# Performance work log

Hardware: AMD Instinct MI355X
Metric: run time of the kernel (lower is better)

Reference implementation:

```python
import jax, jax.numpy as jnp
import numpy as np

# dimensions
B, NQ, D, H, L, KT, KF = 4, 8192, 256, 8, 4, 2, 2
K = KT * KF
DH = D // H
SPATIAL = np.array([[64, 64], [32, 32], [16, 16], [8, 8]], dtype=np.int32)  # (H_l, W_l)
_sizes = SPATIAL[:, 0] * SPATIAL[:, 1]
LSI = np.concatenate([[0], np.cumsum(_sizes)[:-1]]).astype(np.int32)
NV = int(_sizes.sum())


def setup_inputs() -> dict:
    key = jax.random.key(0)
    ks = jax.random.split(key, 12)
    s = 0.02  # small weight scale keeps tanh in linear region like the zero-init original
    # biases per _reset_parameters: +-0.5 grid for offsets, level-specialization for level_weights
    b_time = jnp.asarray(np.tile(np.linspace(-0.5, 0.5, KT), H * L).astype(np.float32))
    b_freq = jnp.asarray(np.tile(np.linspace(-0.5, 0.5, KF).astype(np.float32), H * L))
    lvl_bias = np.zeros((H, L), dtype=np.float32)
    hpl = max(1, H // L)
    for lvl in range(L):
        lvl_bias[lvl * hpl:min(lvl * hpl + hpl, H), lvl] = 1.0
    return dict(
        query=jax.random.normal(ks[0], (B, NQ, D), jnp.float32),
        reference_points=jax.random.uniform(ks[1], (B, NQ, L, 2), jnp.float32),
        value=jax.random.normal(ks[2], (B, NV, D), jnp.float32),
        spatial_shapes=jnp.asarray(SPATIAL),
        level_start_index=jnp.asarray(LSI),
        W_time=jax.random.normal(ks[3], (D, H * L * KT), jnp.float32) * s,
        b_time=b_time,
        W_freq=jax.random.normal(ks[4], (D, H * L * KF), jnp.float32) * s,
        b_freq=b_freq,
        W_lvl=jax.random.normal(ks[5], (D, H * L), jnp.float32) * s,
        b_lvl=jnp.asarray(lvl_bias.reshape(-1)),
        W_pt=jax.random.normal(ks[6], (D, H * L * K), jnp.float32) * s,
        b_pt=jnp.zeros((H * L * K,), jnp.float32),
        W_v=jax.random.normal(ks[7], (D, D), jnp.float32) * (1.0 / np.sqrt(D)),
        b_v=jnp.zeros((D,), jnp.float32),
        W_o=jax.random.normal(ks[8], (D, D), jnp.float32) * (1.0 / np.sqrt(D)),
        b_o=jnp.zeros((D,), jnp.float32),
    )


def _bilinear(vlev, gx, gy, Hl, Wl):
    # vlev: [B,H,Hl*Wl,DH]; gx,gy: [B,H,NQ,K] normalized grid coords in [-1,1]
    # F.grid_sample(align_corners=False, padding_mode='zeros') semantics
    x = (gx + 1.0) * (Wl * 0.5) - 0.5
    y = (gy + 1.0) * (Hl * 0.5) - 0.5
    x0 = jnp.floor(x)
    y0 = jnp.floor(y)
    wx1 = x - x0
    wy1 = y - y0
    x0i = x0.astype(jnp.int32)
    y0i = y0.astype(jnp.int32)

    def gather(xi, yi, w):
        valid = (xi >= 0) & (xi < Wl) & (yi >= 0) & (yi < Hl)
        idx = jnp.clip(yi, 0, Hl - 1) * Wl + jnp.clip(xi, 0, Wl - 1)
        b, h, nq, k = idx.shape
        v = jnp.take_along_axis(vlev, idx.reshape(b, h, nq * k)[..., None], axis=2)
        v = v.reshape(b, h, nq, k, DH)
        return v * (w * valid)[..., None]

    return (gather(x0i, y0i, (1.0 - wx1) * (1.0 - wy1))
            + gather(x0i + 1, y0i, wx1 * (1.0 - wy1))
            + gather(x0i, y0i + 1, (1.0 - wx1) * wy1)
            + gather(x0i + 1, y0i + 1, wx1 * wy1))


def _forward(query, reference_points, value, W_time, b_time, W_freq, b_freq,
             W_lvl, b_lvl, W_pt, b_pt, W_v, b_v, W_o, b_o,
             spatial_shapes, level_start_index):
    ss = np.asarray(spatial_shapes)
    lsi = np.asarray(level_start_index)
    # predicted separable offsets (offset_scale = 1.0)
    t_off = jnp.tanh(query @ W_time + b_time).reshape(B, NQ, H, L, KT)
    f_off = jnp.tanh(query @ W_freq + b_freq).reshape(B, NQ, H, L, KF)
    # square grid: outer product of time (x) and freq (y) offsets -> K = KT*KF points
    off = jnp.stack([
        jnp.broadcast_to(t_off[..., :, None], (B, NQ, H, L, KT, KF)),
        jnp.broadcast_to(f_off[..., None, :], (B, NQ, H, L, KT, KF)),
    ], axis=-1).reshape(B, NQ, H, L, K, 2)
    # normalizer: (W_l, H_l) per level
    norm = jnp.stack([spatial_shapes[:, 1], spatial_shapes[:, 0]], axis=-1).astype(jnp.float32)
    loc = reference_points[:, :, None, :, None, :] + off / norm[None, None, None, :, None, :]
    loc = jnp.clip(loc, 0.0, 1.0)
    grid = 2.0 * loc - 1.0  # [B,NQ,H,L,K,2], last dim = (x, y)
    # attention weights: softmax over levels times softmax over points
    lw = jax.nn.softmax((query @ W_lvl + b_lvl).reshape(B, NQ, H, L), axis=-1)
    pw = jax.nn.softmax((query @ W_pt + b_pt).reshape(B, NQ, H, L, K), axis=-1)
    attn = lw[..., None] * pw  # [B,NQ,H,L,K]
    v = (value @ W_v + b_v).reshape(B, NV, H, DH)
    out = jnp.zeros((B, NQ, H, DH), jnp.float32)
    for lid in range(L):
        Hl, Wl = int(ss[lid, 0]), int(ss[lid, 1])
        start = int(lsi[lid])
        vlev = v[:, start:start + Hl * Wl].transpose(0, 2, 1, 3)  # [B,H,S_l,DH]
        gx = grid[:, :, :, lid, :, 0].transpose(0, 2, 1, 3)  # [B,H,NQ,K]
        gy = grid[:, :, :, lid, :, 1].transpose(0, 2, 1, 3)
        sampled = _bilinear(vlev, gx, gy, Hl, Wl)  # [B,H,NQ,K,DH]
        a = attn[:, :, :, lid, :].transpose(0, 2, 1, 3)  # [B,H,NQ,K]
        out = out + jnp.einsum('bhqkd,bhqk->bqhd', sampled, a)
    out = out.reshape(B, NQ, D)
    return out @ W_o + b_o


def reference(query, reference_points, value, spatial_shapes, level_start_index,
              W_time, b_time, W_freq, b_freq, W_lvl, b_lvl, W_pt, b_pt,
              W_v, b_v, W_o, b_o):
    return _forward(query, reference_points, value, W_time, b_time, W_freq, b_freq,
                    W_lvl, b_lvl, W_pt, b_pt, W_v, b_v, W_o, b_o,
                    spatial_shapes, level_start_index)
```

## Files before the change

kernel.cpp:

```cpp
#include <hip/hip_runtime.h>
#include <math.h>

#define B_  4
#define NQ_ 8192
#define D_  256
#define H_  8
#define L_  4
#define K_  4
#define DH_ 32
#define NV_ 5440

#define SLAB_ 5936

typedef short bf16x8 __attribute__((ext_vector_type(8)));
typedef float f32x4  __attribute__((ext_vector_type(4)));
typedef float f32x8  __attribute__((ext_vector_type(8)));
typedef unsigned short u16x8 __attribute__((ext_vector_type(8)));

__device__ __forceinline__ ushort f2bf(float f) {
    union { float f; unsigned u; } v; v.f = f;
    return (ushort)((v.u + 0x7FFF + ((v.u >> 16) & 1)) >> 16);
}
__device__ __forceinline__ float bf2f(ushort u) {
    union { unsigned u; float f; } v; v.u = ((unsigned)u) << 16;
    return v.f;
}

__global__ __launch_bounds__(256) void k_prep(const float* __restrict__ Wv,
                                              const float* __restrict__ Wo,
                                              const float* __restrict__ Wt,
                                              const float* __restrict__ Wf,
                                              const float* __restrict__ Wlv,
                                              const float* __restrict__ Wp,
                                              uint4* __restrict__ vzero,
                                              ushort* __restrict__ Wvt,
                                              ushort* __restrict__ Wot,
                                              ushort* __restrict__ Wqt) {
    const int bk = blockIdx.x;
    const int t  = threadIdx.x;
    if (bk < 2968) {
        vzero[(size_t)bk * 256 + t] = make_uint4(0, 0, 0, 0);
    } else if (bk < 3480) {
        const float* in; ushort* out; int n;
        if (bk < 3224) { in = Wv; out = Wvt; n = bk - 2968; }
        else           { in = Wo; out = Wot; n = bk - 3224; }
        out[n * 256 + t] = f2bf(in[t * 256 + n]);
    } else {
        const int n = bk - 3480;
        float v;
        if (n < 64)       v = Wt[t * 64 + n];
        else if (n < 128) v = Wf[t * 64 + (n - 64)];
        else if (n < 160) v = Wlv[t * 32 + (n - 128)];
        else              v = Wp[t * 128 + (n - 160)];
        Wqt[n * 256 + t] = f2bf(v);
    }
}

template<int MODE, int AF32>
__global__ __launch_bounds__(256) void k_gemm(const void* __restrict__ Ap,
                                              const ushort* __restrict__ Bt,
                                              const float* __restrict__ bias,
                                              void* __restrict__ Cp) {
    constexpr int NT = 128;
    constexpr int NFN = 4;
    __shared__ ushort As[128 * 32];
    __shared__ ushort Bs[NT * 32];
    const int m0   = blockIdx.x * 128;
    const int n0   = blockIdx.y * NT;
    const int t    = threadIdx.x;
    const int w    = t >> 6;
    const int lane = t & 63;
    const int wm   = (w >> 1) * 64;
    const int wn   = (w & 1) * (NT / 2);
    const int lm   = lane & 15;
    const int quad = lane >> 4;

    f32x4 acc[4][NFN];
    #pragma unroll
    for (int i = 0; i < 4; ++i)
        #pragma unroll
        for (int j = 0; j < NFN; ++j)
            acc[i][j] = (f32x4)(0.f);

    for (int kc = 0; kc < 256; kc += 32) {
        __syncthreads();
        if (AF32) {
            const float* A = (const float*)Ap;
            #pragma unroll
            for (int i = 0; i < 4; ++i) {
                const int c   = t + i * 256;
                const int row = c >> 3, ko = (c & 7) * 4;
                const float4 v = *(const float4*)&A[(size_t)(m0 + row) * 256 + kc + ko];
                ushort4 u; u.x = f2bf(v.x); u.y = f2bf(v.y); u.z = f2bf(v.z); u.w = f2bf(v.w);
                *(ushort4*)&As[row * 32 + ko] = u;
            }
        } else {
            const ushort* A = (const ushort*)Ap;
            #pragma unroll
            for (int i = 0; i < 2; ++i) {
                const int c   = t + i * 256;
                const int row = c >> 2, ko = (c & 3) * 8;
                *(u16x8*)&As[row * 32 + ko] =
                    *(const u16x8*)&A[(size_t)(m0 + row) * 256 + kc + ko];
            }
        }
        #pragma unroll
        for (int i = 0; i < 2; ++i) {
            const int c = t + i * 256;
            const int row = c >> 2, ko = (c & 3) * 8;
            *(u16x8*)&Bs[row * 32 + ko] =
                *(const u16x8*)&Bt[(size_t)(n0 + row) * 256 + kc + ko];
        }
        __syncthreads();

        bf16x8 af[4], bfr[NFN];
        #pragma unroll
        for (int mf = 0; mf < 4; ++mf)
            af[mf] = *(const bf16x8*)&As[(wm + mf * 16 + lm) * 32 + quad * 8];
        #pragma unroll
        for (int nf = 0; nf < NFN; ++nf)
            bfr[nf] = *(const bf16x8*)&Bs[(wn + nf * 16 + lm) * 32 + quad * 8];
        #pragma unroll
        for (int mf = 0; mf < 4; ++mf)
            #pragma unroll
            for (int nf = 0; nf < NFN; ++nf)
                acc[mf][nf] = __builtin_amdgcn_mfma_f32_16x16x32_bf16(
                    af[mf], bfr[nf], acc[mf][nf], 0, 0, 0);
    }

    #pragma unroll
    for (int mf = 0; mf < 4; ++mf) {
        #pragma unroll
        for (int nf = 0; nf < NFN; ++nf) {
            const f32x4 a = acc[mf][nf];
            const int col   = n0 + wn + nf * 16 + lm;
            const int rbase = m0 + wm + mf * 16 + quad * 4;
            #pragma unroll
            for (int r = 0; r < 4; ++r) {
                const int row = rbase + r;
                const float v = a[r];
                if (MODE == 0) {
                    ((float*)Cp)[(size_t)row * 256 + col] = v + bias[col];
                } else {
                    const int b = row / NV_, s = row - b * NV_;
                    const int h = col >> 5, dh = col & 31;
                    const int l = (s >= 5376) ? 3 : (s >= 5120) ? 2 : (s >= 4096) ? 1 : 0;
                    const int lsi_[4] = {0, 4096, 5120, 5376};
                    const int po_[4]  = {0, 4356, 5512, 5836};
                    const int o  = s - lsi_[l];
                    const int Wl = 64 >> l;
                    const int y  = o >> (6 - l);
                    const int x  = o & (Wl - 1);
                    const int prow = po_[l] + (y + 1) * (Wl + 2) + (x + 1);
                    ((ushort*)Cp)[(((size_t)(b * H_ + h)) * SLAB_ + prow) * 32 + dh] =
                        f2bf(v + bias[col]);
                }
            }
        }
    }
}

__global__ __launch_bounds__(256) void k_qproj(const float* __restrict__ query,
                                               const ushort* __restrict__ Wqt,
                                               const float* __restrict__ refpts,
                                               const float* __restrict__ bt,
                                               const float* __restrict__ bfq,
                                               const float* __restrict__ blv,
                                               const float* __restrict__ bp,
                                               float* __restrict__ params) {
    __shared__ __align__(16) char smem[37888];
    ushort* As = (ushort*)smem;
    ushort* Bs = As + 64 * 32;
    float*  ep = (float*)smem;

    const int m0   = blockIdx.x * 64;
    const int t    = threadIdx.x;
    const int w    = t >> 6;
    const int lane = t & 63;
    const int wm   = (w >> 1) * 32;
    const int wn   = (w & 1) * 144;
    const int lm   = lane & 15;
    const int quad = lane >> 4;

    f32x4 acc[2][9];
    #pragma unroll
    for (int i = 0; i < 2; ++i)
        #pragma unroll
        for (int j = 0; j < 9; ++j)
            acc[i][j] = (f32x4)(0.f);

    for (int kc = 0; kc < 256; kc += 32) {
        __syncthreads();
        #pragma unroll
        for (int i = 0; i < 2; ++i) {
            const int c   = t + i * 256;
            const int row = c >> 3, ko = (c & 7) * 4;
            const float4 v = *(const float4*)&query[(size_t)(m0 + row) * 256 + kc + ko];
            ushort4 u; u.x = f2bf(v.x); u.y = f2bf(v.y); u.z = f2bf(v.z); u.w = f2bf(v.w);
            *(ushort4*)&As[row * 32 + ko] = u;
        }
        #pragma unroll
        for (int i = 0; i < 5; ++i) {
            const int c = t + i * 256;
            if (c < 1152) {
                const int row = c >> 2, ko = (c & 3) * 8;
                *(u16x8*)&Bs[row * 32 + ko] =
                    *(const u16x8*)&Wqt[(size_t)row * 256 + kc + ko];
            }
        }
        __syncthreads();

        bf16x8 af[2], bfr[9];
        #pragma unroll
        for (int mf = 0; mf < 2; ++mf)
            af[mf] = *(const bf16x8*)&As[(wm + mf * 16 + lm) * 32 + quad * 8];
        #pragma unroll
        for (int nf = 0; nf < 9; ++nf)
            bfr[nf] = *(const bf16x8*)&Bs[(wn + nf * 16 + lm) * 32 + quad * 8];
        #pragma unroll
        for (int mf = 0; mf < 2; ++mf)
            #pragma unroll
            for (int nf = 0; nf < 9; ++nf)
                acc[mf][nf] = __builtin_amdgcn_mfma_f32_16x16x32_bf16(
                    af[mf], bfr[nf], acc[mf][nf], 0, 0, 0);
    }

    #pragma unroll
    for (int ph = 0; ph < 2; ++ph) {
        __syncthreads();
        if ((w >> 1) == ph) {
            #pragma unroll
            for (int mf = 0; mf < 2; ++mf)
                #pragma unroll
                for (int nf = 0; nf < 9; ++nf)
                    #pragma unroll
                    for (int r = 0; r < 4; ++r)
                        ep[(mf * 16 + quad * 4 + r) * 296 + wn + nf * 16 + lm]
                            = acc[mf][nf][r];
        }
        __syncthreads();
        #pragma unroll
        for (int it = 0; it < 4; ++it) {
            const int item = t + it * 256;
            const int qr = item >> 5;
            const int hl = item & 31;
            const int h = hl >> 2, l = hl & 3;
            const int qg = m0 + ph * 32 + qr;
            const float* lgr = &ep[qr * 296];

            const float tA = tanhf(lgr[hl * 2 + 0] + bt[hl * 2 + 0]);
            const float tB = tanhf(lgr[hl * 2 + 1] + bt[hl * 2 + 1]);
            const float fA = tanhf(lgr[64 + hl * 2 + 0] + bfq[hl * 2 + 0]);
            const float fB = tanhf(lgr[64 + hl * 2 + 1] + bfq[hl * 2 + 1]);

            const float l0 = lgr[128 + h * 4 + 0] + blv[h * 4 + 0];
            const float l1 = lgr[128 + h * 4 + 1] + blv[h * 4 + 1];
            const float l2 = lgr[128 + h * 4 + 2] + blv[h * 4 + 2];
            const float l3 = lgr[128 + h * 4 + 3] + blv[h * 4 + 3];
            const float lmx = fmaxf(fmaxf(l0, l1), fmaxf(l2, l3));
            const float e0 = __expf(l0 - lmx), e1 = __expf(l1 - lmx);
            const float e2 = __expf(l2 - lmx), e3 = __expf(l3 - lmx);
            const float lsum = e0 + e1 + e2 + e3;
            const float lwv = ((l == 0) ? e0 : (l == 1) ? e1 : (l == 2) ? e2 : e3) / lsum;

            const float p0 = lgr[160 + hl * 4 + 0] + bp[hl * 4 + 0];
            const float p1 = lgr[160 + hl * 4 + 1] + bp[hl * 4 + 1];
            const float p2 = lgr[160 + hl * 4 + 2] + bp[hl * 4 + 2];
            const float p3 = lgr[160 + hl * 4 + 3] + bp[hl * 4 + 3];
            const float pmx = fmaxf(fmaxf(p0, p1), fmaxf(p2, p3));
            const float q0e = __expf(p0 - pmx), q1e = __expf(p1 - pmx);
            const float q2e = __expf(p2 - pmx), q3e = __expf(p3 - pmx);
            const float inv = lwv / (q0e + q1e + q2e + q3e);

            const float rx = refpts[((size_t)qg * L_ + l) * 2 + 0];
            const float ry = refpts[((size_t)qg * L_ + l) * 2 + 1];
            const float Wlf = (float)(64 >> l);
            const float Hlf = (float)(64 >> l);
            const float xA = fminf(fmaxf(rx + tA / Wlf, 0.f), 1.f) * Wlf - 0.5f;
            const float xB = fminf(fmaxf(rx + tB / Wlf, 0.f), 1.f) * Wlf - 0.5f;
            const float yA = fminf(fmaxf(ry + fA / Hlf, 0.f), 1.f) * Hlf - 0.5f;
            const float yB = fminf(fmaxf(ry + fB / Hlf, 0.f), 1.f) * Hlf - 0.5f;

            float* pp = params + (size_t)qg * 256 + hl * 8;
            pp[0] = q0e * inv; pp[1] = q1e * inv; pp[2] = q2e * inv; pp[3] = q3e * inv;
            pp[4] = xA; pp[5] = xB; pp[6] = yA; pp[7] = yB;
        }
    }
}

__global__ __launch_bounds__(256) void k_sample(const ushort* __restrict__ vperm,
                                                const float* __restrict__ params,
                                                ushort* __restrict__ mid) {
    __shared__ float pm[8][264];
    const int fid = blockIdx.x;
    const int b   = (fid & 7) >> 1;
    const int q0  = (((fid >> 3) << 1) | (fid & 1)) * 8;
    const int t   = threadIdx.x;
    const int ql  = t >> 5;
    const int sub = t & 31;
    const int h   = sub >> 2;
    const int dh8 = sub & 3;

    for (int i = t; i < 8 * 256; i += 256) {
        const int q = i >> 8, c = i & 255;
        pm[q][(c >> 5) * 33 + (c & 31)] = params[((size_t)(b * NQ_ + q0 + q)) * 256 + c];
    }
    __syncthreads();

    const ushort* vb = vperm + ((size_t)(b * H_ + h)) * SLAB_ * 32 + dh8 * 8;
    const int po_[4] = {0, 4356, 5512, 5836};

    f32x8 acc = (f32x8)(0.f);
    #pragma unroll
    for (int l = 0; l < L_; ++l) {
        const int W2 = (64 >> l) + 2;
        const ushort* vl = vb + (size_t)po_[l] * 32;
        const float* p  = &pm[ql][h * 33 + l * 8];
        const float a0 = p[0], a1 = p[1], a2 = p[2], a3 = p[3];
        const float xA = p[4], xB = p[5], yA = p[6], yB = p[7];
        const float xa0 = floorf(xA), xb0 = floorf(xB);
        const float ya0 = floorf(yA), yb0 = floorf(yB);
        const float fxa = xA - xa0, fxb = xB - xb0;
        const float fya = yA - ya0, fyb = yB - yb0;
        const int pxa = (int)xa0 + 1, pxb = (int)xb0 + 1;
        const int pya = (int)ya0 + 1, pyb = (int)yb0 + 1;
        #pragma unroll
        for (int k = 0; k < 4; ++k) {
            const int   px = (k & 2) ? pxb : pxa;
            const int   py = (k & 1) ? pyb : pya;
            const float fx = (k & 2) ? fxb : fxa;
            const float fy = (k & 1) ? fyb : fya;
            const float ak = (k == 0) ? a0 : (k == 1) ? a1 : (k == 2) ? a2 : a3;
            const ushort* cp = vl + (size_t)(py * W2 + px) * 32;
            const u16x8 u00 = *(const u16x8*)cp;
            const u16x8 u10 = *(const u16x8*)(cp + 32);
            const u16x8 u01 = *(const u16x8*)(cp + W2 * 32);
            const u16x8 u11 = *(const u16x8*)(cp + (W2 + 1) * 32);
            const float gx = 1.f - fx, gy = 1.f - fy;
            const float w00 = ak * gx * gy, w10 = ak * fx * gy;
            const float w01 = ak * gx * fy, w11 = ak * fx * fy;
            #pragma unroll
            for (int e = 0; e < 8; ++e)
                acc[e] += bf2f(u00[e]) * w00 + bf2f(u10[e]) * w10
                        + bf2f(u01[e]) * w01 + bf2f(u11[e]) * w11;
        }
    }
    u16x8 o;
    #pragma unroll
    for (int e = 0; e < 8; ++e) o[e] = f2bf(acc[e]);
    *(u16x8*)&mid[((size_t)(b * NQ_ + q0 + ql)) * 256 + sub * 8] = o;
}

extern "C" void kernel_launch(void* const* d_in, const int* in_sizes, int n_in,
                              void* d_out, int out_size, void* d_ws, size_t ws_size,
                              hipStream_t stream) {
    const float* query = (const float*)d_in[0];
    const float* refp  = (const float*)d_in[1];
    const float* value = (const float*)d_in[2];
    const float* Wt = (const float*)d_in[5];
    const float* bt = (const float*)d_in[6];
    const float* Wf = (const float*)d_in[7];
    const float* bf = (const float*)d_in[8];
    const float* Wl = (const float*)d_in[9];
    const float* bl = (const float*)d_in[10];
    const float* Wp = (const float*)d_in[11];
    const float* bp = (const float*)d_in[12];
    const float* Wv = (const float*)d_in[13];
    const float* bv = (const float*)d_in[14];
    const float* Wo = (const float*)d_in[15];
    const float* bo = (const float*)d_in[16];

    char* wsb = (char*)d_ws;
    ushort* vperm  = (ushort*)wsb;
    float*  params = (float*)(wsb + 12156928);
    ushort* midb   = (ushort*)(wsb + 45711360);
    ushort* Wvt    = (ushort*)(wsb + 62488576);
    ushort* Wot    = (ushort*)(wsb + 62619648);
    ushort* Wqt    = (ushort*)(wsb + 62750720);

    k_prep<<<3768, 256, 0, stream>>>(Wv, Wo, Wt, Wf, Wl, Wp,
                                     (uint4*)vperm, Wvt, Wot, Wqt);
    k_gemm<1, 1><<<dim3(170, 2), 256, 0, stream>>>(value, Wvt, bv, vperm);
    k_qproj<<<512, 256, 0, stream>>>(query, Wqt, refp, bt, bf, bl, bp, params);
    k_sample<<<dim3(NQ_ / 8 * B_), 256, 0, stream>>>(vperm, params, midb);
    k_gemm<0, 0><<<dim3(256, 2), 256, 0, stream>>>(midb, Wot, bo, (float*)d_out);
}
```

Measured before the change: 232.8 us.

## Double-buffer GEMM and query-projection tiles with direct global-to-LDS loads

Both the generic GEMM kernel and the query-projection kernel now keep two LDS buffers and prefetch the next K-chunk while the MFMAs run on the current one. Bf16 operands are copied straight into LDS with the global_load_lds builtin, and fp32 operands are held in registers, then converted and written after the MFMAs. This cuts one barrier per iteration and hides global load latency behind compute. The cost is more LDS and registers, which can lower occupancy, plus reliance on the direct-to-LDS instruction placing data in the expected layout without an explicit wait.

```diff
diff --git a/kernel.cpp b/kernel.cpp
--- a/kernel.cpp
+++ b/kernel.cpp
@@ -24,6 +24,11 @@
 __device__ __forceinline__ float bf2f(ushort u) {
     union { unsigned u; float f; } v; v.u = ((unsigned)u) << 16;
     return v.f;
+}
+__device__ __forceinline__ void gld16(const void* g, void* l) {
+    __builtin_amdgcn_global_load_lds(
+        (const __attribute__((address_space(1))) unsigned int*)g,
+        (__attribute__((address_space(3))) unsigned int*)l, 16, 0, 0);
 }
 
 __global__ __launch_bounds__(256) void k_prep(const float* __restrict__ Wv,
@@ -61,77 +66,106 @@
                                               const ushort* __restrict__ Bt,
                                               const float* __restrict__ bias,
                                               void* __restrict__ Cp) {
-    constexpr int NT = 128;
-    constexpr int NFN = 4;
-    __shared__ ushort As[128 * 32];
-    __shared__ ushort Bs[NT * 32];
+    __shared__ __align__(16) ushort As[2][128 * 32];
+    __shared__ __align__(16) ushort Bs[2][128 * 32];
     const int m0   = blockIdx.x * 128;
-    const int n0   = blockIdx.y * NT;
+    const int n0   = blockIdx.y * 128;
     const int t    = threadIdx.x;
     const int w    = t >> 6;
     const int lane = t & 63;
     const int wm   = (w >> 1) * 64;
-    const int wn   = (w & 1) * (NT / 2);
+    const int wn   = (w & 1) * 64;
     const int lm   = lane & 15;
     const int quad = lane >> 4;
 
-    f32x4 acc[4][NFN];
+    float4 areg[4];
+
+    auto stageB = [&](int buf, int kc) {
+        #pragma unroll
+        for (int i = 0; i < 2; ++i) {
+            const int c0 = (i * 4 + w) * 64;
+            const int c  = c0 + lane;
+            const int row = c >> 2, ko = (c & 3) * 8;
+            gld16(&Bt[(size_t)(n0 + row) * 256 + kc + ko],
+                  (ushort*)&Bs[buf][0] + (size_t)c0 * 8);
+        }
+    };
+    auto stageA16 = [&](int buf, int kc) {
+        const ushort* A = (const ushort*)Ap;
+        #pragma unroll
+        for (int i = 0; i < 2; ++i) {
+            const int c0 = (i * 4 + w) * 64;
+            const int c  = c0 + lane;
+            const int row = c >> 2, ko = (c & 3) * 8;
+            gld16(&A[(size_t)(m0 + row) * 256 + kc + ko],
+                  (ushort*)&As[buf][0] + (size_t)c0 * 8);
+        }
+    };
+    auto loadA32 = [&](int kc) {
+        const float* A = (const float*)Ap;
+        #pragma unroll
+        for (int i = 0; i < 4; ++i) {
+            const int c = t + i * 256;
+            const int row = c >> 3, ko = (c & 7) * 4;
+            areg[i] = *(const float4*)&A[(size_t)(m0 + row) * 256 + kc + ko];
+        }
+    };
+    auto writeA32 = [&](int buf) {
+        #pragma unroll
+        for (int i = 0; i < 4; ++i) {
+            const int c = t + i * 256;
+            const int row = c >> 3, ko = (c & 7) * 4;
+            ushort4 u;
+            u.x = f2bf(areg[i].x); u.y = f2bf(areg[i].y);
+            u.z = f2bf(areg[i].z); u.w = f2bf(areg[i].w);
+            *(ushort4*)&As[buf][row * 32 + ko] = u;
+        }
+    };
+
+    f32x4 acc[4][4];
     #pragma unroll
     for (int i = 0; i < 4; ++i)
         #pragma unroll
-        for (int j = 0; j < NFN; ++j)
+        for (int j = 0; j < 4; ++j)
             acc[i][j] = (f32x4)(0.f);
 
+    if (AF32) { loadA32(0); writeA32(0); }
+    else      { stageA16(0, 0); }
+    stageB(0, 0);
+    __syncthreads();
+
+    int cur = 0;
     for (int kc = 0; kc < 256; kc += 32) {
-        __syncthreads();
-        if (AF32) {
-            const float* A = (const float*)Ap;
-            #pragma unroll
-            for (int i = 0; i < 4; ++i) {
-                const int c   = t + i * 256;
-                const int row = c >> 3, ko = (c & 7) * 4;
-                const float4 v = *(const float4*)&A[(size_t)(m0 + row) * 256 + kc + ko];
-                ushort4 u; u.x = f2bf(v.x); u.y = f2bf(v.y); u.z = f2bf(v.z); u.w = f2bf(v.w);
-                *(ushort4*)&As[row * 32 + ko] = u;
-            }
-        } else {
-            const ushort* A = (const ushort*)Ap;
-            #pragma unroll
-            for (int i = 0; i < 2; ++i) {
-                const int c   = t + i * 256;
-                const int row = c >> 2, ko = (c & 3) * 8;
-                *(u16x8*)&As[row * 32 + ko] =
-                    *(const u16x8*)&A[(size_t)(m0 + row) * 256 + kc + ko];
-            }
-        }
-        #pragma unroll
-        for (int i = 0; i < 2; ++i) {
-            const int c = t + i * 256;
-            const int row = c >> 2, ko = (c & 3) * 8;
-            *(u16x8*)&Bs[row * 32 + ko] =
-                *(const u16x8*)&Bt[(size_t)(n0 + row) * 256 + kc + ko];
-        }
-        __syncthreads();
-
-        bf16x8 af[4], bfr[NFN];
+        const int nxt = cur ^ 1;
+        bf16x8 af[4], bfr[4];
         #pragma unroll
         for (int mf = 0; mf < 4; ++mf)
-            af[mf] = *(const bf16x8*)&As[(wm + mf * 16 + lm) * 32 + quad * 8];
-        #pragma unroll
-        for (int nf = 0; nf < NFN; ++nf)
-            bfr[nf] = *(const bf16x8*)&Bs[(wn + nf * 16 + lm) * 32 + quad * 8];
+            af[mf] = *(const bf16x8*)&As[cur][(wm + mf * 16 + lm) * 32 + quad * 8];
+        #pragma unroll
+        for (int nf = 0; nf < 4; ++nf)
+            bfr[nf] = *(const bf16x8*)&Bs[cur][(wn + nf * 16 + lm) * 32 + quad * 8];
+        if (kc + 32 < 256) {
+            if (AF32) loadA32(kc + 32);
+            else      stageA16(nxt, kc + 32);
+            stageB(nxt, kc + 32);
+        }
         #pragma unroll
         for (int mf = 0; mf < 4; ++mf)
             #pragma unroll
-            for (int nf = 0; nf < NFN; ++nf)
+            for (int nf = 0; nf < 4; ++nf)
                 acc[mf][nf] = __builtin_amdgcn_mfma_f32_16x16x32_bf16(
                     af[mf], bfr[nf], acc[mf][nf], 0, 0, 0);
+        if (kc + 32 < 256) {
+            if (AF32) writeA32(nxt);
+            __syncthreads();
+        }
+        cur = nxt;
     }
 
     #pragma unroll
     for (int mf = 0; mf < 4; ++mf) {
         #pragma unroll
-        for (int nf = 0; nf < NFN; ++nf) {
+        for (int nf = 0; nf < 4; ++nf) {
             const f32x4 a = acc[mf][nf];
             const int col   = n0 + wn + nf * 16 + lm;
             const int rbase = m0 + wm + mf * 16 + quad * 4;
@@ -168,10 +202,10 @@
                                                const float* __restrict__ blv,
                                                const float* __restrict__ bp,
                                                float* __restrict__ params) {
-    __shared__ __align__(16) char smem[37888];
-    ushort* As = (ushort*)smem;
-    ushort* Bs = As + 64 * 32;
-    float*  ep = (float*)smem;
+    __shared__ __align__(16) char smem[45056];
+    ushort* As0 = (ushort*)smem;
+    ushort* Bs0 = (ushort*)(smem + 8192);
+    float*  ep  = (float*)smem;
 
     const int m0   = blockIdx.x * 64;
     const int t    = threadIdx.x;
@@ -182,6 +216,42 @@
     const int lm   = lane & 15;
     const int quad = lane >> 4;
 
+    float4 areg[2];
+
+    auto stageB = [&](int buf, int kc) {
+        ushort* B = Bs0 + buf * 9216;
+        #pragma unroll
+        for (int i = 0; i < 5; ++i) {
+            const int cb = i * 4 + w;
+            if (cb < 18) {
+                const int c0 = cb * 64;
+                const int c  = c0 + lane;
+                const int row = c >> 2, ko = (c & 3) * 8;
+                gld16(&Wqt[(size_t)row * 256 + kc + ko], B + (size_t)c0 * 8);
+            }
+        }
+    };
+    auto loadA = [&](int kc) {
+        #pragma unroll
+        for (int i = 0; i < 2; ++i) {
+            const int c = t + i * 256;
+            const int row = c >> 3, ko = (c & 7) * 4;
+            areg[i] = *(const float4*)&query[(size_t)(m0 + row) * 256 + kc + ko];
+        }
+    };
+    auto writeA = [&](int buf) {
+        ushort* A = As0 + buf * 2048;
+        #pragma unroll
+        for (int i = 0; i < 2; ++i) {
+            const int c = t + i * 256;
+            const int row = c >> 3, ko = (c & 7) * 4;
+            ushort4 u;
+            u.x = f2bf(areg[i].x); u.y = f2bf(areg[i].y);
+            u.z = f2bf(areg[i].z); u.w = f2bf(areg[i].w);
+            *(ushort4*)&A[row * 32 + ko] = u;
+        }
+    };
+
     f32x4 acc[2][9];
     #pragma unroll
     for (int i = 0; i < 2; ++i)
@@ -189,40 +259,37 @@
         for (int j = 0; j < 9; ++j)
             acc[i][j] = (f32x4)(0.f);
 
+    loadA(0); writeA(0);
+    stageB(0, 0);
+    __syncthreads();
+
+    int cur = 0;
     for (int kc = 0; kc < 256; kc += 32) {
-        __syncthreads();
-        #pragma unroll
-        for (int i = 0; i < 2; ++i) {
-            const int c   = t + i * 256;
-            const int row = c >> 3, ko = (c & 7) * 4;
-            const float4 v = *(const float4*)&query[(size_t)(m0 + row) * 256 + kc + ko];
-            ushort4 u; u.x = f2bf(v.x); u.y = f2bf(v.y); u.z = f2bf(v.z); u.w = f2bf(v.w);
-            *(ushort4*)&As[row * 32 + ko] = u;
-        }
-        #pragma unroll
-        for (int i = 0; i < 5; ++i) {
-            const int c = t + i * 256;
-            if (c < 1152) {
-                const int row = c >> 2, ko = (c & 3) * 8;
-                *(u16x8*)&Bs[row * 32 + ko] =
-                    *(const u16x8*)&Wqt[(size_t)row * 256 + kc + ko];
-            }
-        }
-        __syncthreads();
-
+        const int nxt = cur ^ 1;
+        const ushort* Ac = As0 + cur * 2048;
+        const ushort* Bc = Bs0 + cur * 9216;
         bf16x8 af[2], bfr[9];
         #pragma unroll
         for (int mf = 0; mf < 2; ++mf)
-            af[mf] = *(const bf16x8*)&As[(wm + mf * 16 + lm) * 32 + quad * 8];
+            af[mf] = *(const bf16x8*)&Ac[(wm + mf * 16 + lm) * 32 + quad * 8];
         #pragma unroll
         for (int nf = 0; nf < 9; ++nf)
-            bfr[nf] = *(const bf16x8*)&Bs[(wn + nf * 16 + lm) * 32 + quad * 8];
+            bfr[nf] = *(const bf16x8*)&Bc[(wn + nf * 16 + lm) * 32 + quad * 8];
+        if (kc + 32 < 256) {
+            loadA(kc + 32);
+            stageB(nxt, kc + 32);
+        }
         #pragma unroll
         for (int mf = 0; mf < 2; ++mf)
             #pragma unroll
             for (int nf = 0; nf < 9; ++nf)
                 acc[mf][nf] = __builtin_amdgcn_mfma_f32_16x16x32_bf16(
                     af[mf], bfr[nf], acc[mf][nf], 0, 0, 0);
+        if (kc + 32 < 256) {
+            writeA(nxt);
+            __syncthreads();
+        }
+        cur = nxt;
     }
 
     #pragma unroll
```

New measurement: 222.4 us. 1.05x faster.
